# Optimization experiments

Measured on AMD Instinct MI355X. Metric: run time of the kernel, lower is better.

The kernel has to match this reference:

```python
import jax, jax.numpy as jnp
import numpy as np
from jax import lax

DIM = 1024
D_STATE = 64
D_CONV = 4
EXPAND = 2
HEADDIM = 64
D_INNER = EXPAND * DIM            # 2048
NHEADS = D_INNER // HEADDIM       # 32
NGROUPS = 1
CONV_DIM = D_INNER + 2 * NGROUPS * D_STATE      # 2176
D_IN_PROJ = 2 * D_INNER + 2 * NGROUPS * D_STATE + NHEADS  # 4256
BATCH, SEQLEN = 2, 4096
EPS = 1e-5


def setup_inputs() -> dict:
    key = jax.random.key(0)
    ks = jax.random.split(key, 10)
    X = jax.random.normal(ks[0], (BATCH, SEQLEN, DIM), dtype=jnp.float32)
    in_proj_w = jax.random.normal(ks[1], (D_IN_PROJ, DIM), dtype=jnp.float32) * 0.02
    conv_w = jax.random.normal(ks[2], (CONV_DIM, 1, D_CONV), dtype=jnp.float32) * 0.2
    conv_b = jax.random.normal(ks[3], (CONV_DIM,), dtype=jnp.float32) * 0.02
    dt_bias = jax.random.normal(ks[4], (NHEADS,), dtype=jnp.float32) * 0.5 - 2.0
    A_log = jnp.log(jax.random.uniform(ks[5], (NHEADS,), minval=1.0, maxval=16.0))
    D = jax.random.normal(ks[6], (NHEADS,), dtype=jnp.float32)
    norm_w = jnp.ones((D_INNER,), dtype=jnp.float32)
    out_proj_w = jax.random.normal(ks[7], (DIM, D_INNER), dtype=jnp.float32) * 0.02
    to_h_w = jax.random.normal(ks[8], (2 * DIM, DIM), dtype=jnp.float32) * 0.02
    return dict(X=X, in_proj_w=in_proj_w, conv_w=conv_w, conv_b=conv_b,
                dt_bias=dt_bias, A_log=A_log, D=D, norm_w=norm_w,
                out_proj_w=out_proj_w, to_h_w=to_h_w)


def _silu(x):
    return x * jax.nn.sigmoid(x)


def _mamba2(X, in_proj_w, conv_w, conv_b, dt_bias, A_log, D, norm_w, out_proj_w):
    Bsz, L, _ = X.shape
    zxbcdt = jnp.einsum('bld,ed->ble', X, in_proj_w)  # (B,L,D_IN_PROJ)
    z = zxbcdt[..., :D_INNER]
    xBC = zxbcdt[..., D_INNER:D_INNER + CONV_DIM]
    dt_raw = zxbcdt[..., D_INNER + CONV_DIM:]
    dt = jax.nn.softplus(dt_raw + dt_bias)  # (B,L,H)

    # causal depthwise conv over time, then silu
    xc = jnp.transpose(xBC, (0, 2, 1))                       # (B,C,L)
    xc = jnp.pad(xc, ((0, 0), (0, 0), (D_CONV - 1, 0)))
    xc = lax.conv_general_dilated(xc, conv_w, window_strides=(1,), padding='VALID',
                                  dimension_numbers=('NCH', 'OIH', 'NCH'),
                                  feature_group_count=CONV_DIM)
    xc = xc + conv_b[None, :, None]
    xBC = _silu(jnp.transpose(xc, (0, 2, 1)))                # (B,L,C)

    x = xBC[..., :D_INNER].reshape(Bsz, L, NHEADS, HEADDIM)  # (B,L,H,P)
    Bm = xBC[..., D_INNER:D_INNER + D_STATE]                 # (B,L,N) ngroups=1
    Cm = xBC[..., D_INNER + D_STATE:]                        # (B,L,N)

    A = -jnp.exp(A_log)                                      # (H,)

    def step(h, inp):
        dt_t, B_t, C_t, x_t = inp   # (B,H), (B,N), (B,N), (B,H,P)
        dA = jnp.exp(dt_t * A)                               # (B,H)
        h = h * dA[..., None, None] + jnp.einsum('bh,bhp,bn->bhpn', dt_t, x_t, B_t)
        y_t = jnp.einsum('bhpn,bn->bhp', h, C_t)
        return h, y_t

    h0 = jnp.zeros((Bsz, NHEADS, HEADDIM, D_STATE), dtype=X.dtype)
    xs = (jnp.moveaxis(dt, 1, 0), jnp.moveaxis(Bm, 1, 0),
          jnp.moveaxis(Cm, 1, 0), jnp.moveaxis(x, 1, 0))
    _, ys = lax.scan(step, h0, xs)                           # (L,B,H,P)
    y = jnp.moveaxis(ys, 0, 1) + x * D[None, None, :, None]  # skip term
    y = y.reshape(Bsz, L, D_INNER)

    # gated RMSNorm: rmsnorm(y * silu(z)) * weight
    y = y * _silu(z)
    y = y * lax.rsqrt(jnp.mean(y * y, axis=-1, keepdims=True) + EPS) * norm_w
    return jnp.einsum('bld,ed->ble', y, out_proj_w)          # (B,L,DIM)


def reference(X, in_proj_w, conv_w, conv_b, dt_bias, A_log, D, norm_w, out_proj_w, to_h_w):
    H = _mamba2(X, in_proj_w, conv_w, conv_b, dt_bias, A_log, D, norm_w, out_proj_w)
    HKV = jnp.einsum('bld,ed->ble', H, to_h_w)               # (B,L,2*DIM)
    HK, HV = HKV[..., :DIM], HKV[..., DIM:]
    return (HK, HV)
```

## Files before the change

### kernel.cpp

```cpp
#include <hip/hip_runtime.h>
#include <hip/hip_bf16.h>
#include <math.h>

#define B_       2
#define L_       4096
#define DIM_     1024
#define DINNER_  2048
#define DSTATE_  64
#define NH_      32
#define HD_      64
#define CONVDIM_ 2176
#define DIP_     4256
#define M_       (B_*L_)
#define XRW_     2208
#define NC_      64

typedef __attribute__((ext_vector_type(8))) short short8;
typedef __attribute__((ext_vector_type(4))) float floatx4;
typedef __hip_bfloat16 bf16;

__device__ __forceinline__ float bf2f(unsigned short u) {
    unsigned int v = ((unsigned int)u) << 16;
    return __builtin_bit_cast(float, v);
}
__device__ __forceinline__ unsigned short f2bf(float f) {
    unsigned int x = __builtin_bit_cast(unsigned int, f);
    unsigned int lsb = (x >> 16) & 1u;
    x += 0x7fffu + lsb;
    return (unsigned short)(x >> 16);
}
__device__ __forceinline__ void storeo(bf16* p, float v) {
    *reinterpret_cast<unsigned short*>(p) = f2bf(v);
}
__device__ __forceinline__ void storeo(float* p, float v) { *p = v; }

__device__ __forceinline__ void gl2lds16(const bf16* g, short* lds) {
    __builtin_amdgcn_global_load_lds(
        (const __attribute__((address_space(1))) void*)g,
        (__attribute__((address_space(3))) void*)lds, 16, 0, 0);
}

__global__ __launch_bounds__(256) void cast_f32_bf16_k(
    const float* __restrict__ src, bf16* __restrict__ dst)
{
    size_t i0 = ((size_t)blockIdx.x * 256 + threadIdx.x) * 8;
    uint4 a = *reinterpret_cast<const uint4*>(src + i0);
    uint4 b = *reinterpret_cast<const uint4*>(src + i0 + 4);
    unsigned int w0 = (unsigned int)f2bf(__builtin_bit_cast(float, a.x)) |
                      ((unsigned int)f2bf(__builtin_bit_cast(float, a.y)) << 16);
    unsigned int w1 = (unsigned int)f2bf(__builtin_bit_cast(float, a.z)) |
                      ((unsigned int)f2bf(__builtin_bit_cast(float, a.w)) << 16);
    unsigned int w2 = (unsigned int)f2bf(__builtin_bit_cast(float, b.x)) |
                      ((unsigned int)f2bf(__builtin_bit_cast(float, b.y)) << 16);
    unsigned int w3 = (unsigned int)f2bf(__builtin_bit_cast(float, b.z)) |
                      ((unsigned int)f2bf(__builtin_bit_cast(float, b.w)) << 16);
    *reinterpret_cast<uint4*>(reinterpret_cast<unsigned short*>(dst) + i0) =
        make_uint4(w0, w1, w2, w3);
}

template <typename TO>
__global__ __launch_bounds__(256) void gemm_bt16(
    const bf16* __restrict__ A, const bf16* __restrict__ W,
    TO* __restrict__ outA, TO* __restrict__ outB,
    int M, int N, int K, int split, int strideA, int strideB)
{
    __shared__ short As[128*64];
    __shared__ short Ws[128*64];
    const int tid  = threadIdx.x;
    const int m0   = blockIdx.y * 128;
    const int n0   = blockIdx.x * 128;
    const int wave = tid >> 6;
    const int lane = tid & 63;
    const int wm   = (wave >> 1) * 64;
    const int wn   = (wave & 1) * 64;
    const int ln   = lane & 15;
    const int quad = lane >> 4;
    const int lr   = lane >> 3;
    const int lc   = (lane & 7) * 8;

    floatx4 acc[4][4];
#pragma unroll
    for (int i = 0; i < 4; i++)
#pragma unroll
        for (int j = 0; j < 4; j++) acc[i][j] = (floatx4){0.f, 0.f, 0.f, 0.f};

    for (int k0 = 0; k0 < K; k0 += 64) {
#pragma unroll
        for (int it = 0; it < 4; it++) {
            int ig = wave * 4 + it;
            gl2lds16(A + (size_t)(m0 + ig * 8 + lr) * K + k0 + lc, &As[ig * 512]);
            gl2lds16(W + (size_t)(n0 + ig * 8 + lr) * K + k0 + lc, &Ws[ig * 512]);
        }
        __syncthreads();
#pragma unroll
        for (int kk = 0; kk < 64; kk += 32) {
            short8 af[4], bfv[4];
#pragma unroll
            for (int i = 0; i < 4; i++)
                af[i] = *reinterpret_cast<const short8*>(&As[(wm + i * 16 + ln) * 64 + kk + quad * 8]);
#pragma unroll
            for (int j = 0; j < 4; j++)
                bfv[j] = *reinterpret_cast<const short8*>(&Ws[(wn + j * 16 + ln) * 64 + kk + quad * 8]);
#pragma unroll
            for (int i = 0; i < 4; i++)
#pragma unroll
                for (int j = 0; j < 4; j++)
                    acc[i][j] = __builtin_amdgcn_mfma_f32_16x16x32_bf16(af[i], bfv[j], acc[i][j], 0, 0, 0);
        }
        __syncthreads();
    }

#pragma unroll
    for (int i = 0; i < 4; i++)
#pragma unroll
        for (int j = 0; j < 4; j++)
#pragma unroll
            for (int r = 0; r < 4; r++) {
                int grow = m0 + wm + i * 16 + quad * 4 + r;
                int gcol = n0 + wn + j * 16 + ln;
                if (gcol < N) {
                    if (gcol < split)
                        storeo(outA + (size_t)grow * strideA + gcol, acc[i][j][r]);
                    else
                        storeo(outB + (size_t)grow * strideB + (gcol - split), acc[i][j][r]);
                }
            }
}

__global__ __launch_bounds__(256) void conv_all_k(
    const bf16* __restrict__ xr, const float* __restrict__ cw,
    const float* __restrict__ cb, bf16* __restrict__ xc)
{
    int idx = blockIdx.x * 256 + threadIdx.x;
    int row = idx / 272;
    int ch0 = (idx - row * 272) * 8;
    int t   = row & (L_ - 1);
    const unsigned short* xru = (const unsigned short*)xr;
    uint4 rv[4];
#pragma unroll
    for (int j = 0; j < 4; j++) {
        rv[j] = make_uint4(0u, 0u, 0u, 0u);
        if (t + j - 3 >= 0)
            rv[j] = *reinterpret_cast<const uint4*>(xru + (size_t)(row + j - 3) * XRW_ + ch0);
    }
    unsigned int ow[4];
#pragma unroll
    for (int pair = 0; pair < 4; pair++) {
        unsigned short o2[2];
#pragma unroll
        for (int k = 0; k < 2; k++) {
            int cc = pair * 2 + k;
            float a = cb[ch0 + cc];
#pragma unroll
            for (int j = 0; j < 4; j++) {
                unsigned int w32 = (&rv[j].x)[cc >> 1];
                unsigned short u = (cc & 1) ? (unsigned short)(w32 >> 16)
                                            : (unsigned short)(w32 & 0xffffu);
                a = fmaf(bf2f(u), cw[(ch0 + cc) * 4 + j], a);
            }
            o2[k] = f2bf(a / (1.f + __expf(-a)));
        }
        ow[pair] = (unsigned int)o2[0] | ((unsigned int)o2[1] << 16);
    }
    *reinterpret_cast<uint4*>((unsigned short*)xc + (size_t)row * CONVDIM_ + ch0) =
        make_uint4(ow[0], ow[1], ow[2], ow[3]);
}

__global__ __launch_bounds__(256) void dt_k(
    const bf16* __restrict__ xr, const float* __restrict__ dtb, float* __restrict__ dtf)
{
    int idx = blockIdx.x * 256 + threadIdx.x;
    int h  = idx & (NH_ - 1);
    int ml = idx >> 5;
    float v = bf2f(((const unsigned short*)xr)[(size_t)ml * XRW_ + 2176 + h]) + dtb[h];
    dtf[idx] = fmaxf(v, 0.f) + log1pf(__expf(-fabsf(v)));
}

__global__ __launch_bounds__(256) void chunk_intra_k(
    const bf16* __restrict__ xc, const float* __restrict__ dtf,
    const float* __restrict__ A_log, const float* __restrict__ Dp,
    bf16* __restrict__ Yg, float* __restrict__ Sg, float* __restrict__ Eg)
{
    __shared__ short Bst[64*72];
    __shared__ short Cst[64*72];
    __shared__ short xsM[64*72];
    __shared__ short xT [64*72];
    __shared__ short BwT[64*72];
    __shared__ float dts[64], cums[64], wS[64];

    const int tid  = threadIdx.x;
    const int bid  = blockIdx.x;
    const int h    = bid & 31;
    const int bc   = bid >> 5;
    const int c    = bc & 63;
    const int b    = bc >> 6;
    const int xch0 = h * 64;
    const unsigned short* xcu = (const unsigned short*)xc;

    const float Ah = -__expf(A_log[h]);
    const float Dh = Dp[h];

    for (int q = tid; q < 1536; q += 256) {
        int sel = q >> 9;
        int qq  = q & 511;
        int r = qq >> 3, c8 = (qq & 7) * 8;
        size_t ro = (size_t)(b * L_ + c * 64 + r) * CONVDIM_;
        if (sel == 0)
            *reinterpret_cast<uint4*>(&Bst[r*72 + c8]) =
                *reinterpret_cast<const uint4*>(xcu + ro + 2048 + c8);
        else if (sel == 1)
            *reinterpret_cast<uint4*>(&Cst[r*72 + c8]) =
                *reinterpret_cast<const uint4*>(xcu + ro + 2112 + c8);
        else
            *reinterpret_cast<uint4*>(&xsM[r*72 + c8]) =
                *reinterpret_cast<const uint4*>(xcu + ro + xch0 + c8);
    }
    if (tid < 64) dts[tid] = dtf[(size_t)(b * L_ + c * 64 + tid) * NH_ + h];
    __syncthreads();

    if (tid == 0) {
        float cc = 0.f;
        for (int t = 0; t < 64; t++) { cc += dts[t] * Ah; cums[t] = cc; }
    }
    __syncthreads();
    if (tid < 64) wS[tid] = __expf(cums[63] - cums[tid]) * dts[tid];
    if (tid == 0) Eg[bid] = __expf(cums[63]);
    __syncthreads();

    for (int q = tid; q < 4096; q += 256) {
        int s = q & 63, ch = q >> 6;
        xT [ch*72 + s] = xsM[s*72 + ch];
        BwT[ch*72 + s] = (short)f2bf(bf2f((unsigned short)Bst[s*72 + ch]) * wS[s]);
    }
    __syncthreads();

    const int wave = tid >> 6, lane = tid & 63;
    const int ln = lane & 15, quad = lane >> 4;
    const int wm = (wave >> 1) * 32, wn = (wave & 1) * 32;

    floatx4 accG[2][2];
#pragma unroll
    for (int i = 0; i < 2; i++)
#pragma unroll
        for (int j = 0; j < 2; j++) accG[i][j] = (floatx4){0.f,0.f,0.f,0.f};
#pragma unroll
    for (int kk = 0; kk < 64; kk += 32) {
        short8 af[2], bfv[2];
#pragma unroll
        for (int i = 0; i < 2; i++)
            af[i] = *reinterpret_cast<const short8*>(&Cst[(wm + i*16 + ln)*72 + kk + quad*8]);
#pragma unroll
        for (int j = 0; j < 2; j++)
            bfv[j] = *reinterpret_cast<const short8*>(&Bst[(wn + j*16 + ln)*72 + kk + quad*8]);
#pragma unroll
        for (int i = 0; i < 2; i++)
#pragma unroll
            for (int j = 0; j < 2; j++)
                accG[i][j] = __builtin_amdgcn_mfma_f32_16x16x32_bf16(af[i], bfv[j], accG[i][j], 0,0,0);
    }
    __syncthreads();
#pragma unroll
    for (int i = 0; i < 2; i++)
#pragma unroll
        for (int j = 0; j < 2; j++)
#pragma unroll
            for (int r = 0; r < 4; r++) {
                int t = wm + i*16 + quad*4 + r;
                int s = wn + j*16 + ln;
                float v = (s <= t) ? __expf(cums[t] - cums[s]) * dts[s] * accG[i][j][r] : 0.f;
                xsM[t*72 + s] = (short)f2bf(v);
            }
    __syncthreads();

    floatx4 accY[2][2];
#pragma unroll
    for (int i = 0; i < 2; i++)
#pragma unroll
        for (int j = 0; j < 2; j++) accY[i][j] = (floatx4){0.f,0.f,0.f,0.f};
#pragma unroll
    for (int kk = 0; kk < 64; kk += 32) {
        short8 af[2], bfv[2];
#pragma unroll
        for (int i = 0; i < 2; i++)
            af[i] = *reinterpret_cast<const short8*>(&xsM[(wm + i*16 + ln)*72 + kk + quad*8]);
#pragma unroll
        for (int j = 0; j < 2; j++)
            bfv[j] = *reinterpret_cast<const short8*>(&xT[(wn + j*16 + ln)*72 + kk + quad*8]);
#pragma unroll
        for (int i = 0; i < 2; i++)
#pragma unroll
            for (int j = 0; j < 2; j++)
                accY[i][j] = __builtin_amdgcn_mfma_f32_16x16x32_bf16(af[i], bfv[j], accY[i][j], 0,0,0);
    }
    unsigned short* Yu = (unsigned short*)Yg;
#pragma unroll
    for (int i = 0; i < 2; i++)
#pragma unroll
        for (int j = 0; j < 2; j++)
#pragma unroll
            for (int r = 0; r < 4; r++) {
                int t = wm + i*16 + quad*4 + r;
                int p = wn + j*16 + ln;
                float yv = accY[i][j][r] + Dh * bf2f((unsigned short)xT[p*72 + t]);
                Yu[(size_t)(b*L_ + c*64 + t)*DINNER_ + xch0 + p] = f2bf(yv);
            }

    floatx4 accS[2][2];
#pragma unroll
    for (int i = 0; i < 2; i++)
#pragma unroll
        for (int j = 0; j < 2; j++) accS[i][j] = (floatx4){0.f,0.f,0.f,0.f};
#pragma unroll
    for (int kk = 0; kk < 64; kk += 32) {
        short8 af[2], bfv[2];
#pragma unroll
        for (int i = 0; i < 2; i++)
            af[i] = *reinterpret_cast<const short8*>(&xT[(wm + i*16 + ln)*72 + kk + quad*8]);
#pragma unroll
        for (int j = 0; j < 2; j++)
            bfv[j] = *reinterpret_cast<const short8*>(&BwT[(wn + j*16 + ln)*72 + kk + quad*8]);
#pragma unroll
        for (int i = 0; i < 2; i++)
#pragma unroll
            for (int j = 0; j < 2; j++)
                accS[i][j] = __builtin_amdgcn_mfma_f32_16x16x32_bf16(af[i], bfv[j], accS[i][j], 0,0,0);
    }
#pragma unroll
    for (int i = 0; i < 2; i++)
#pragma unroll
        for (int j = 0; j < 2; j++)
#pragma unroll
            for (int r = 0; r < 4; r++) {
                int p = wm + i*16 + quad*4 + r;
                int n = wn + j*16 + ln;
                Sg[(size_t)bid * 4096 + p*64 + n] = accS[i][j][r];
            }
}

__global__ __launch_bounds__(256) void chunk_state_k(
    float* __restrict__ Sg, const float* __restrict__ Eg)
{
    int g  = blockIdx.x * 1024 + threadIdx.x * 4;
    int bh = g >> 12;
    int b  = bh >> 5, h = bh & 31;
    int e  = g & 4095;
    float4 run = make_float4(0.f, 0.f, 0.f, 0.f);
    for (int c = 0; c < NC_; c++) {
        int bid = (b * 64 + c) * 32 + h;
        size_t idx = (size_t)bid * 4096 + e;
        float4 s = *reinterpret_cast<float4*>(&Sg[idx]);
        float  E = Eg[bid];
        *reinterpret_cast<float4*>(&Sg[idx]) = run;
        run.x = run.x * E + s.x;
        run.y = run.y * E + s.y;
        run.z = run.z * E + s.z;
        run.w = run.w * E + s.w;
    }
}

__global__ __launch_bounds__(256) void chunk_inter_k(
    const bf16* __restrict__ xc, const float* __restrict__ Sg,
    const float* __restrict__ dtf, const float* __restrict__ A_log,
    bf16* __restrict__ Yg)
{
    __shared__ short Cst[64*72];
    __shared__ short hpT[64*72];
    __shared__ float dts[64], cums[64], wcumL[64];

    const int tid = threadIdx.x;
    const int bid = blockIdx.x;
    const int h   = bid & 31;
    const int bc  = bid >> 5;
    const int c   = bc & 63;
    const int b   = bc >> 6;
    const unsigned short* xcu = (const unsigned short*)xc;

    const float Ah = -__expf(A_log[h]);

    for (int q = tid; q < 512; q += 256) {
        int r = q >> 3, c8 = (q & 7) * 8;
        *reinterpret_cast<uint4*>(&Cst[r*72 + c8]) =
            *reinterpret_cast<const uint4*>(xcu + (size_t)(b*L_ + c*64 + r)*CONVDIM_ + 2112 + c8);
    }
    for (int q = tid; q < 1024; q += 256) {
        int p = q >> 4, n4 = (q & 15) * 4;
        float4 v = *reinterpret_cast<const float4*>(&Sg[(size_t)bid * 4096 + p*64 + n4]);
        unsigned int lo = (unsigned int)f2bf(v.x) | ((unsigned int)f2bf(v.y) << 16);
        unsigned int hi = (unsigned int)f2bf(v.z) | ((unsigned int)f2bf(v.w) << 16);
        *reinterpret_cast<uint2*>(&hpT[p*72 + n4]) = make_uint2(lo, hi);
    }
    if (tid < 64) dts[tid] = dtf[(size_t)(b*L_ + c*64 + tid) * NH_ + h];
    __syncthreads();
    if (tid == 0) {
        float cc = 0.f;
        for (int t = 0; t < 64; t++) { cc += dts[t] * Ah; cums[t] = cc; }
    }
    __syncthreads();
    if (tid < 64) wcumL[tid] = __expf(cums[tid]);
    __syncthreads();

    const int wave = tid >> 6, lane = tid & 63;
    const int ln = lane & 15, quad = lane >> 4;
    const int wm = (wave >> 1) * 32, wn = (wave & 1) * 32;

    floatx4 acc[2][2];
#pragma unroll
    for (int i = 0; i < 2; i++)
#pragma unroll
        for (int j = 0; j < 2; j++) acc[i][j] = (floatx4){0.f,0.f,0.f,0.f};
#pragma unroll
    for (int kk = 0; kk < 64; kk += 32) {
        short8 af[2], bfv[2];
#pragma unroll
        for (int i = 0; i < 2; i++)
            af[i] = *reinterpret_cast<const short8*>(&Cst[(wm + i*16 + ln)*72 + kk + quad*8]);
#pragma unroll
        for (int j = 0; j < 2; j++)
            bfv[j] = *reinterpret_cast<const short8*>(&hpT[(wn + j*16 + ln)*72 + kk + quad*8]);
#pragma unroll
        for (int i = 0; i < 2; i++)
#pragma unroll
            for (int j = 0; j < 2; j++)
                acc[i][j] = __builtin_amdgcn_mfma_f32_16x16x32_bf16(af[i], bfv[j], acc[i][j], 0,0,0);
    }
    unsigned short* Yu = (unsigned short*)Yg;
#pragma unroll
    for (int i = 0; i < 2; i++)
#pragma unroll
        for (int j = 0; j < 2; j++)
#pragma unroll
            for (int r = 0; r < 4; r++) {
                int t = wm + i*16 + quad*4 + r;
                int p = wn + j*16 + ln;
                size_t idx = (size_t)(b*L_ + c*64 + t)*DINNER_ + h*64 + p;
                float yv = bf2f(Yu[idx]) + wcumL[t] * acc[i][j][r];
                Yu[idx] = f2bf(yv);
            }
}

__global__ __launch_bounds__(256) void gate_norm_k(
    bf16* __restrict__ y, const bf16* __restrict__ zbuf, const float* __restrict__ nw)
{
    __shared__ float red[4];
    int row = blockIdx.x;
    int tid = threadIdx.x;
    unsigned short* yy = (unsigned short*)y;
    const unsigned short* zz = (const unsigned short*)zbuf;

    uint4 yv = *reinterpret_cast<uint4*>(&yy[(size_t)row * DINNER_ + tid * 8]);
    uint4 zv = *reinterpret_cast<const uint4*>(&zz[(size_t)row * DINNER_ + tid * 8]);
    unsigned int yw[4] = {yv.x, yv.y, yv.z, yv.w};
    unsigned int zw[4] = {zv.x, zv.y, zv.z, zv.w};
    float g[8];
    float ss = 0.f;
#pragma unroll
    for (int q = 0; q < 4; q++) {
        float y0 = bf2f((unsigned short)(yw[q] & 0xffffu)), y1 = bf2f((unsigned short)(yw[q] >> 16));
        float z0 = bf2f((unsigned short)(zw[q] & 0xffffu)), z1 = bf2f((unsigned short)(zw[q] >> 16));
        float g0 = y0 * (z0 / (1.f + __expf(-z0)));
        float g1 = y1 * (z1 / (1.f + __expf(-z1)));
        g[q * 2] = g0; g[q * 2 + 1] = g1;
        ss += g0 * g0 + g1 * g1;
    }
#pragma unroll
    for (int o = 1; o < 64; o <<= 1) ss += __shfl_xor(ss, o);
    if ((tid & 63) == 0) red[tid >> 6] = ss;
    __syncthreads();
    float tot = red[0] + red[1] + red[2] + red[3];
    float rinv = rsqrtf(tot * (1.f / DINNER_) + 1e-5f);

    unsigned int ow[4];
#pragma unroll
    for (int q = 0; q < 4; q++) {
        float w0 = nw[tid * 8 + q * 2];
        float w1 = nw[tid * 8 + q * 2 + 1];
        unsigned short o0 = f2bf(g[q * 2] * rinv * w0);
        unsigned short o1 = f2bf(g[q * 2 + 1] * rinv * w1);
        ow[q] = (unsigned int)o0 | ((unsigned int)o1 << 16);
    }
    *reinterpret_cast<uint4*>(&yy[(size_t)row * DINNER_ + tid * 8]) =
        make_uint4(ow[0], ow[1], ow[2], ow[3]);
}


extern "C" void kernel_launch(void* const* d_in, const int* in_sizes, int n_in,
                              void* d_out, int out_size, void* d_ws, size_t ws_size,
                              hipStream_t stream)
{
    const float* X    = (const float*)d_in[0];
    const float* Wip  = (const float*)d_in[1];
    const float* cw   = (const float*)d_in[2];
    const float* cb   = (const float*)d_in[3];
    const float* dtb  = (const float*)d_in[4];
    const float* Alog = (const float*)d_in[5];
    const float* Dp   = (const float*)d_in[6];
    const float* nw   = (const float*)d_in[7];
    const float* Wop  = (const float*)d_in[8];
    const float* Wth  = (const float*)d_in[9];
    float* out = (float*)d_out;

    char* ws = (char*)d_ws;
    bf16*  zbuf = (bf16*) (ws);
    bf16*  Wopb = (bf16*) (ws);
    bf16*  Wthb = (bf16*) (ws + 4194304);
    bf16*  xr   = (bf16*) (ws + 33554432);
    bf16*  Yg   = (bf16*) (ws + 33554432);
    bf16*  xc   = (bf16*) (ws + 69730304);
    bf16*  Xb   = (bf16*) (ws + 69730304);
    bf16*  Wipb = (bf16*) (ws + 69730304 + 16777216);
    bf16*  Hbuf = (bf16*) (ws + 69730304);
    float* dtf  = (float*)(ws + 105381888);
    float* Eg   = (float*)(ws + 106430464);
    float* Sg   = (float*)d_out;

    dim3 blk(256);

    cast_f32_bf16_k<<<(M_ * DIM_) / 2048, blk, 0, stream>>>(X, Xb);
    cast_f32_bf16_k<<<(DIP_ * DIM_) / 2048, blk, 0, stream>>>(Wip, Wipb);

    gemm_bt16<bf16><<<dim3(34, M_ / 128), blk, 0, stream>>>(
        Xb, Wipb, zbuf, xr, M_, DIP_, DIM_, DINNER_, DINNER_, XRW_);

    dt_k<<<(M_ * NH_) / 256, blk, 0, stream>>>(xr, dtb, dtf);
    conv_all_k<<<(M_ * 272) / 256, blk, 0, stream>>>(xr, cw, cb, xc);

    chunk_intra_k<<<B_ * NC_ * NH_, blk, 0, stream>>>(
        xc, dtf, Alog, Dp, Yg, Sg, Eg);
    chunk_state_k<<<256, blk, 0, stream>>>(Sg, Eg);
    chunk_inter_k<<<B_ * NC_ * NH_, blk, 0, stream>>>(xc, Sg, dtf, Alog, Yg);

    gate_norm_k<<<M_, blk, 0, stream>>>(Yg, zbuf, nw);

    cast_f32_bf16_k<<<(DIM_ * DINNER_) / 2048, blk, 0, stream>>>(Wop, Wopb);
    cast_f32_bf16_k<<<(DINNER_ * DIM_) / 2048, blk, 0, stream>>>(Wth, Wthb);

    gemm_bt16<bf16><<<dim3(DIM_ / 128, M_ / 128), blk, 0, stream>>>(
        Yg, Wopb, Hbuf, Hbuf, M_, DIM_, DINNER_, DIM_, DIM_, DIM_);

    gemm_bt16<float><<<dim3(DINNER_ / 128, M_ / 128), blk, 0, stream>>>(
        Hbuf, Wthb, out, out + (size_t)M_ * DIM_, M_, DINNER_, DIM_, DIM_, DIM_, DIM_);
}
```

Measured before the change: 511.6 us.

## Replace GEMM with 256x256 double-buffered swizzled LDS kernel and XCD block remap

Replaces the 128x128 single-buffered bf16 MFMA GEMM with a 512-thread, 256x256-tile kernel. It double-buffers the LDS and interleaves global-to-LDS prefetch of the next K slice with MFMA on the current one. It also XOR-swizzles LDS addresses to reduce bank conflicts, remaps the 1D grid so neighbouring tiles land on the same XCD, and raises wave priority around the MFMA bursts. The aim is more data reuse per LDS load and hiding global-load latency. In exchange it uses 128 KB of LDS per block, so occupancy is low, and it launches few blocks for the smaller GEMMs, leaving the tail poorly balanced.

```diff
diff --git a/kernel.cpp b/kernel.cpp
--- a/kernel.cpp
+++ b/kernel.cpp
@@ -59,72 +59,147 @@
 }
 
 template <typename TO>
-__global__ __launch_bounds__(256) void gemm_bt16(
-    const bf16* __restrict__ A, const bf16* __restrict__ W,
+__global__ __launch_bounds__(512, 2) void gemm256(
+    const bf16* __restrict__ Ag, const bf16* __restrict__ Wg,
     TO* __restrict__ outA, TO* __restrict__ outB,
-    int M, int N, int K, int split, int strideA, int strideB)
-{
-    __shared__ short As[128*64];
-    __shared__ short Ws[128*64];
+    int M, int N, int K, int split, int strideA, int strideB, int nbx)
+{
+    __shared__ short lds[65536];
+
     const int tid  = threadIdx.x;
-    const int m0   = blockIdx.y * 128;
-    const int n0   = blockIdx.x * 128;
     const int wave = tid >> 6;
     const int lane = tid & 63;
-    const int wm   = (wave >> 1) * 64;
-    const int wn   = (wave & 1) * 64;
     const int ln   = lane & 15;
     const int quad = lane >> 4;
-    const int lr   = lane >> 3;
-    const int lc   = (lane & 7) * 8;
-
-    floatx4 acc[4][4];
+    const int wr   = wave >> 2;
+    const int wc   = wave & 3;
+    const int bh   = wc >> 1;
+    const int wcl  = wc & 1;
+    const int xorv = ((ln >> 2) & 1) << 5;
+
+    int nwg  = gridDim.x;
+    int orig = blockIdx.x;
+    int wg   = ((nwg & 7) == 0) ? ((orig & 7) * (nwg >> 3) + (orig >> 3)) : orig;
+    const int bx = wg % nbx;
+    const int by = wg / nbx;
+    const int m0 = by * 256;
+    const int n0 = bx * 256;
+
+    int lo0 = tid * 16;
+    int lo1 = 8192 + tid * 16;
+    int so0 = lo0 ^ (((lo0 >> 9) & 1) << 5);
+    int so1 = lo1 ^ (((lo1 >> 9) & 1) << 5);
+    const int srow0 = so0 >> 7, scol0 = (so0 & 127) >> 1;
+    const int srow1 = so1 >> 7, scol1 = (so1 & 127) >> 1;
+
+#define STG_A(bufb, h, kc) do {                                               \
+    short* dst_ = &lds[((bufb)*2 + (h)) * 8192 + wave * 512];                 \
+    gl2lds16(Ag + (size_t)(m0 + (h)*128 + srow0) * K + (kc) + scol0, dst_);   \
+    gl2lds16(Ag + (size_t)(m0 + (h)*128 + srow1) * K + (kc) + scol1, dst_ + 4096); \
+} while (0)
+#define STG_B(bufb, h, kc) do {                                               \
+    short* dst_ = &lds[32768 + ((bufb)*2 + (h)) * 8192 + wave * 512];         \
+    gl2lds16(Wg + (size_t)(n0 + (h)*128 + srow0) * K + (kc) + scol0, dst_);   \
+    gl2lds16(Wg + (size_t)(n0 + (h)*128 + srow1) * K + (kc) + scol1, dst_ + 4096); \
+} while (0)
+
+#define RD_A(qi) do {                                                         \
+    const char* Ab_ = (const char*)&lds[(cur*2 + wr) * 8192];                 \
+    _Pragma("unroll") for (int i = 0; i < 4; i++)                             \
+    _Pragma("unroll") for (int ks = 0; ks < 2; ks++)                          \
+        af[i][ks] = *reinterpret_cast<const short8*>(                         \
+            Ab_ + ((((qi)*64 + i*16 + ln)*128 + ks*64 + quad*16) ^ xorv));    \
+} while (0)
+#define RD_B(qj) do {                                                         \
+    const char* Bb_ = (const char*)&lds[32768 + (cur*2 + bh) * 8192];         \
+    _Pragma("unroll") for (int j = 0; j < 2; j++)                             \
+    _Pragma("unroll") for (int ks = 0; ks < 2; ks++)                          \
+        bfv[j][ks] = *reinterpret_cast<const short8*>(                        \
+            Bb_ + (((wcl*64 + (qj)*32 + j*16 + ln)*128 + ks*64 + quad*16) ^ xorv)); \
+} while (0)
+
+#define MMA(qi, qj) do {                                                      \
+    __builtin_amdgcn_s_setprio(1);                                            \
+    _Pragma("unroll") for (int i = 0; i < 4; i++)                             \
+    _Pragma("unroll") for (int j = 0; j < 2; j++)                             \
+    _Pragma("unroll") for (int ks = 0; ks < 2; ks++)                          \
+        acc[(qi)*4+i][(qj)*2+j] = __builtin_amdgcn_mfma_f32_16x16x32_bf16(    \
+            af[i][ks], bfv[j][ks], acc[(qi)*4+i][(qj)*2+j], 0, 0, 0);         \
+    __builtin_amdgcn_s_setprio(0);                                            \
+} while (0)
+
+    floatx4 acc[8][4];
+#pragma unroll
+    for (int i = 0; i < 8; i++)
+#pragma unroll
+        for (int j = 0; j < 4; j++) acc[i][j] = (floatx4){0.f, 0.f, 0.f, 0.f};
+
+    const int NT = K >> 6;
+
+    STG_A(0, 0, 0); STG_A(0, 1, 0);
+    STG_B(0, 0, 0); STG_B(0, 1, 0);
+    asm volatile("s_waitcnt vmcnt(0)" ::: "memory");
+    __builtin_amdgcn_s_barrier();
+    __builtin_amdgcn_sched_barrier(0);
+
+    short8 af[4][2], bfv[2][2];
+
+    for (int t = 0; t < NT; ++t) {
+        const int cur = t & 1, nxt = cur ^ 1;
+        const int kc  = (t + 1) << 6;
+        const bool pf = (t + 1 < NT);
+
+        if (pf) { STG_A(nxt, 0, kc); STG_A(nxt, 1, kc); }
+        RD_A(0); RD_B(0);
+        __builtin_amdgcn_s_barrier();
+        MMA(0, 0);
+        __builtin_amdgcn_s_barrier();
+
+        if (pf) { STG_B(nxt, 0, kc); STG_B(nxt, 1, kc); }
+        RD_B(1);
+        __builtin_amdgcn_s_barrier();
+        MMA(0, 1);
+        __builtin_amdgcn_s_barrier();
+
+        RD_A(1); RD_B(0);
+        __builtin_amdgcn_s_barrier();
+        MMA(1, 0);
+        __builtin_amdgcn_s_barrier();
+
+        RD_B(1);
+        __builtin_amdgcn_s_barrier();
+        MMA(1, 1);
+        if (pf) { asm volatile("s_waitcnt vmcnt(0)" ::: "memory"); }
+        __builtin_amdgcn_s_barrier();
+        __builtin_amdgcn_sched_barrier(0);
+    }
+
+#undef STG_A
+#undef STG_B
+#undef RD_A
+#undef RD_B
+#undef MMA
+
+#pragma unroll
+    for (int qi = 0; qi < 2; qi++)
 #pragma unroll
     for (int i = 0; i < 4; i++)
 #pragma unroll
-        for (int j = 0; j < 4; j++) acc[i][j] = (floatx4){0.f, 0.f, 0.f, 0.f};
-
-    for (int k0 = 0; k0 < K; k0 += 64) {
-#pragma unroll
-        for (int it = 0; it < 4; it++) {
-            int ig = wave * 4 + it;
-            gl2lds16(A + (size_t)(m0 + ig * 8 + lr) * K + k0 + lc, &As[ig * 512]);
-            gl2lds16(W + (size_t)(n0 + ig * 8 + lr) * K + k0 + lc, &Ws[ig * 512]);
+    for (int qj = 0; qj < 2; qj++)
+#pragma unroll
+    for (int j = 0; j < 2; j++)
+#pragma unroll
+    for (int r = 0; r < 4; r++) {
+        int grow = m0 + wr*128 + qi*64 + i*16 + quad*4 + r;
+        int gcol = n0 + wc*64 + qj*32 + j*16 + ln;
+        float v = acc[qi*4+i][qj*2+j][r];
+        if (gcol < N) {
+            if (gcol < split)
+                storeo(outA + (size_t)grow * strideA + gcol, v);
+            else
+                storeo(outB + (size_t)grow * strideB + (gcol - split), v);
         }
-        __syncthreads();
-#pragma unroll
-        for (int kk = 0; kk < 64; kk += 32) {
-            short8 af[4], bfv[4];
-#pragma unroll
-            for (int i = 0; i < 4; i++)
-                af[i] = *reinterpret_cast<const short8*>(&As[(wm + i * 16 + ln) * 64 + kk + quad * 8]);
-#pragma unroll
-            for (int j = 0; j < 4; j++)
-                bfv[j] = *reinterpret_cast<const short8*>(&Ws[(wn + j * 16 + ln) * 64 + kk + quad * 8]);
-#pragma unroll
-            for (int i = 0; i < 4; i++)
-#pragma unroll
-                for (int j = 0; j < 4; j++)
-                    acc[i][j] = __builtin_amdgcn_mfma_f32_16x16x32_bf16(af[i], bfv[j], acc[i][j], 0, 0, 0);
-        }
-        __syncthreads();
-    }
-
-#pragma unroll
-    for (int i = 0; i < 4; i++)
-#pragma unroll
-        for (int j = 0; j < 4; j++)
-#pragma unroll
-            for (int r = 0; r < 4; r++) {
-                int grow = m0 + wm + i * 16 + quad * 4 + r;
-                int gcol = n0 + wn + j * 16 + ln;
-                if (gcol < N) {
-                    if (gcol < split)
-                        storeo(outA + (size_t)grow * strideA + gcol, acc[i][j][r]);
-                    else
-                        storeo(outB + (size_t)grow * strideB + (gcol - split), acc[i][j][r]);
-                }
-            }
+    }
 }
 
 __global__ __launch_bounds__(256) void conv_all_k(
@@ -514,12 +589,13 @@
     float* Sg   = (float*)d_out;
 
     dim3 blk(256);
+    dim3 blk512(512);
 
     cast_f32_bf16_k<<<(M_ * DIM_) / 2048, blk, 0, stream>>>(X, Xb);
     cast_f32_bf16_k<<<(DIP_ * DIM_) / 2048, blk, 0, stream>>>(Wip, Wipb);
 
-    gemm_bt16<bf16><<<dim3(34, M_ / 128), blk, 0, stream>>>(
-        Xb, Wipb, zbuf, xr, M_, DIP_, DIM_, DINNER_, DINNER_, XRW_);
+    gemm256<bf16><<<dim3(17 * 32), blk512, 0, stream>>>(
+        Xb, Wipb, zbuf, xr, M_, DIP_, DIM_, DINNER_, DINNER_, XRW_, 17);
 
     dt_k<<<(M_ * NH_) / 256, blk, 0, stream>>>(xr, dtb, dtf);
     conv_all_k<<<(M_ * 272) / 256, blk, 0, stream>>>(xr, cw, cb, xc);
@@ -534,9 +610,9 @@
     cast_f32_bf16_k<<<(DIM_ * DINNER_) / 2048, blk, 0, stream>>>(Wop, Wopb);
     cast_f32_bf16_k<<<(DINNER_ * DIM_) / 2048, blk, 0, stream>>>(Wth, Wthb);
 
-    gemm_bt16<bf16><<<dim3(DIM_ / 128, M_ / 128), blk, 0, stream>>>(
-        Yg, Wopb, Hbuf, Hbuf, M_, DIM_, DINNER_, DIM_, DIM_, DIM_);
-
-    gemm_bt16<float><<<dim3(DINNER_ / 128, M_ / 128), blk, 0, stream>>>(
-        Hbuf, Wthb, out, out + (size_t)M_ * DIM_, M_, DINNER_, DIM_, DIM_, DIM_, DIM_);
-}
+    gemm256<bf16><<<dim3(4 * 32), blk512, 0, stream>>>(
+        Yg, Wopb, Hbuf, Hbuf, M_, DIM_, DINNER_, DIM_, DIM_, DIM_, 4);
+
+    gemm256<float><<<dim3(8 * 32), blk512, 0, stream>>>(
+        Hbuf, Wthb, out, out + (size_t)M_ * DIM_, M_, DINNER_, DIM_, DIM_, DIM_, DIM_, 8);
+}
```

New measurement: 517.4 us. About the same (+1.1%).
